# Optimization experiments

Measured on AMD Instinct MI355X. Metric: run time of the kernel, lower is better.

The kernel has to match this reference:

```python
import jax, jax.numpy as jnp
import numpy as np

B, T, H, L2 = 131072, 4, 8, 5  # T=4 forced by conv1 in_channels=4; L2 = layers 1..5 of the 6-layer lstm1


def _lstm_dir(xs, w_ih, w_hh, b, h0, c0):
    # xs: [T, B, Din] -> hs: [T, B, H]; PyTorch gate order i, f, g, o
    def step(carry, xt):
        h, c = carry
        g = xt @ w_ih.T + h @ w_hh.T + b
        i, f, gg, o = jnp.split(g, 4, axis=-1)
        c = jax.nn.sigmoid(f) * c + jax.nn.sigmoid(i) * jnp.tanh(gg)
        h = jax.nn.sigmoid(o) * jnp.tanh(c)
        return (h, c), h
    _, hs = jax.lax.scan(step, (h0, c0), xs)
    return hs


def _bilstm(xs, wi_f, wh_f, b_f, wi_b, wh_b, b_b, h0f, c0f, h0b, c0b):
    hf = _lstm_dir(xs, wi_f, wh_f, b_f, h0f, c0f)
    hb = _lstm_dir(xs[::-1], wi_b, wh_b, b_b, h0b, c0b)[::-1]
    return jnp.concatenate([hf, hb], axis=-1)  # [T, B, 2H]


def _conv1d(x, w, b):
    # x: [B, C, L], w: [O, I, K] (torch Conv1d layout)
    y = jax.lax.conv_general_dilated(x, w, (1,), [(0, 0)], dimension_numbers=('NCH', 'OIH', 'NCH'))
    return y + b[None, :, None]


def _deconv1d(x, w, b):
    # torch ConvTranspose1d weight [I, O, K]; stride 1, pad 0 == full conv with flipped kernel
    k = w.shape[-1]
    wk = jnp.flip(jnp.swapaxes(w, 0, 1), -1)  # [O, I, K]
    y = jax.lax.conv_general_dilated(x, wk, (1,), [(k - 1, k - 1)], dimension_numbers=('NCH', 'OIH', 'NCH'))
    return y + b[None, :, None]


def setup_inputs():
    key = jax.random.key(0)
    ks = iter(jax.random.split(key, 32))
    rn = lambda shape, s=0.2: jax.random.normal(next(ks), shape, jnp.float32) * s
    return {
        'x': rn((B, T, 2), 1.0),
        'h0': rn((12, B, H), 1.0),
        'c0': rn((12, B, H), 1.0),
        'w_ih0': rn((2, 4 * H, 2)),
        'w_hh0': rn((2, 4 * H, H)),
        'b_ih0': rn((2, 4 * H)),
        'b_hh0': rn((2, 4 * H)),
        'w_ih': rn((L2, 2, 4 * H, 2 * H)),
        'w_hh': rn((L2, 2, 4 * H, H)),
        'b_ih': rn((L2, 2, 4 * H)),
        'b_hh': rn((L2, 2, 4 * H)),
        'conv1_w': rn((8, 4, 2)), 'conv1_b': rn((8,)),
        'conv2_w': rn((16, 8, 2)), 'conv2_b': rn((16,)),
        'deconv1_w': rn((16, 8, 2)), 'deconv1_b': rn((8,)),
        'deconv2_w': rn((8, 4, 2)), 'deconv2_b': rn((4,)),
        'fc1_w': rn((8, 16)), 'fc1_b': rn((8,)),
        'fc2_w': rn((4, 8)), 'fc2_b': rn((4,)),
    }


def reference(x, h0, c0, w_ih0, w_hh0, b_ih0, b_hh0, w_ih, w_hh, b_ih, b_hh,
              conv1_w, conv1_b, conv2_w, conv2_b, deconv1_w, deconv1_b,
              deconv2_w, deconv2_b, fc1_w, fc1_b, fc2_w, fc2_b):
    xs = jnp.swapaxes(x, 0, 1)  # [T, B, 2]
    y = _bilstm(xs, w_ih0[0], w_hh0[0], b_ih0[0] + b_hh0[0],
                w_ih0[1], w_hh0[1], b_ih0[1] + b_hh0[1],
                h0[0], c0[0], h0[1], c0[1])
    for l in range(L2):  # fixed, small layer count (eval mode: inter-layer dropout off)
        i = 2 * (l + 1)
        y = _bilstm(y, w_ih[l, 0], w_hh[l, 0], b_ih[l, 0] + b_hh[l, 0],
                    w_ih[l, 1], w_hh[l, 1], b_ih[l, 1] + b_hh[l, 1],
                    h0[i], c0[i], h0[i + 1], c0[i + 1])
    y = jax.nn.sigmoid(jnp.swapaxes(y, 0, 1))  # [B, 4, 16]; dim 1 acts as conv channels
    y = _conv1d(y, conv1_w, conv1_b)           # [B, 8, 15]
    y = _conv1d(y, conv2_w, conv2_b)           # [B, 16, 14]
    y = _deconv1d(y, deconv1_w, deconv1_b)     # [B, 8, 15]
    y = _deconv1d(y, deconv2_w, deconv2_b)     # [B, 4, 16]
    y = y @ fc1_w.T + fc1_b                    # [B, 4, 8]
    y = y @ fc2_w.T + fc2_b                    # [B, 4, 4]
    return jnp.tanh(y)
```

## Files before the change

### kernel.cpp

```cpp
#include <hip/hip_runtime.h>
#include <hip/hip_bf16.h>


using f32x2 = __attribute__((ext_vector_type(2))) float;
using f32x4 = __attribute__((ext_vector_type(4))) float;

#define OFF_WIH0 0
#define OFF_WHH0 128
#define OFF_B0   640
#define OFF_WIH  704
#define OFF_WHH  5824
#define OFF_B    8384
#define OFF_M    9024
#define OFF_MB   10048

__device__ __forceinline__ float rcpf_(float x) {
#if __has_builtin(__builtin_amdgcn_rcpf)
    return __builtin_amdgcn_rcpf(x);
#else
    return 1.0f / x;
#endif
}
__device__ __forceinline__ float exp2f_(float x) {
#if __has_builtin(__builtin_amdgcn_exp2f)
    return __builtin_amdgcn_exp2f(x);
#else
    return exp2f(x);
#endif
}
__device__ __forceinline__ float sigm(float x) {
    return rcpf_(1.0f + exp2f_(-1.44269504f * x));
}
__device__ __forceinline__ float tanhx(float x) {
    return fmaf(2.0f, rcpf_(1.0f + exp2f_(-2.88539008f * x)), -1.0f);
}

__global__ __launch_bounds__(256) void prep_all(
    const float* __restrict__ wih0, const float* __restrict__ whh0,
    const float* __restrict__ bih0, const float* __restrict__ bhh0,
    const float* __restrict__ wih,  const float* __restrict__ whh,
    const float* __restrict__ bih,  const float* __restrict__ bhh,
    const float* __restrict__ c1w, const float* __restrict__ c1b,
    const float* __restrict__ c2w, const float* __restrict__ c2b,
    const float* __restrict__ d1w, const float* __restrict__ d1b,
    const float* __restrict__ d2w, const float* __restrict__ d2b,
    const float* __restrict__ f1w, const float* __restrict__ f1b,
    const float* __restrict__ f2w, const float* __restrict__ f2b,
    float* __restrict__ W)
{
    __shared__ float A[13][232];
    __shared__ float Bf[13][232];
    const int tid = threadIdx.x;

    if (blockIdx.x < 36) {
        int t = blockIdx.x * 256 + tid;
        const int n = 36 * 256;
        for (int i = t; i < 128; i += n)  W[OFF_WIH0 + i] = wih0[i];
        for (int i = t; i < 512; i += n)  W[OFF_WHH0 + i] = whh0[i];
        for (int i = t; i < 64; i += n)   W[OFF_B0 + i] = bih0[i] + bhh0[i];
        for (int i = t; i < 5120; i += n) W[OFF_WIH + i] = wih[i];
        for (int i = t; i < 2560; i += n) W[OFF_WHH + i] = whh[i];
        for (int i = t; i < 640; i += n)  W[OFF_B + i] = bih[i] + bhh[i];
        return;
    }
    const int base = (blockIdx.x - 36) * 13;

    for (int idx = tid; idx < 13 * 64; idx += 256) {
        int cl = idx / 64, r = idx % 64;
        A[cl][r] = (base + cl == r) ? 1.0f : 0.0f;
    }
    __syncthreads();
    for (int idx = tid; idx < 13 * 120; idx += 256) {
        int cl = idx / 120, rr = idx % 120; int o = rr / 15, l = rr % 15;
        float acc = (base + cl == 64) ? c1b[o] : 0.0f;
        for (int i = 0; i < 4; i++)
            for (int kk = 0; kk < 2; kk++)
                acc += c1w[(o * 4 + i) * 2 + kk] * A[cl][i * 16 + l + kk];
        Bf[cl][rr] = acc;
    }
    __syncthreads();
    for (int idx = tid; idx < 13 * 224; idx += 256) {
        int cl = idx / 224, rr = idx % 224; int o = rr / 14, l = rr % 14;
        float acc = (base + cl == 64) ? c2b[o] : 0.0f;
        for (int i = 0; i < 8; i++)
            for (int kk = 0; kk < 2; kk++)
                acc += c2w[(o * 8 + i) * 2 + kk] * Bf[cl][i * 15 + l + kk];
        A[cl][rr] = acc;
    }
    __syncthreads();
    for (int idx = tid; idx < 13 * 120; idx += 256) {
        int cl = idx / 120, rr = idx % 120; int o = rr / 15, l = rr % 15;
        float acc = (base + cl == 64) ? d1b[o] : 0.0f;
        for (int i = 0; i < 16; i++)
            for (int kk = 0; kk < 2; kk++) {
                int ls = l - kk;
                if (ls >= 0 && ls < 14)
                    acc += d1w[(i * 8 + o) * 2 + kk] * A[cl][i * 14 + ls];
            }
        Bf[cl][rr] = acc;
    }
    __syncthreads();
    for (int idx = tid; idx < 13 * 64; idx += 256) {
        int cl = idx / 64, rr = idx % 64; int o = rr / 16, l = rr % 16;
        float acc = (base + cl == 64) ? d2b[o] : 0.0f;
        for (int i = 0; i < 8; i++)
            for (int kk = 0; kk < 2; kk++) {
                int ls = l - kk;
                if (ls >= 0 && ls < 15)
                    acc += d2w[(i * 4 + o) * 2 + kk] * Bf[cl][i * 15 + ls];
            }
        A[cl][rr] = acc;
    }
    __syncthreads();
    for (int idx = tid; idx < 13 * 32; idx += 256) {
        int cl = idx / 32, rr = idx % 32; int ch = rr / 8, jj = rr % 8;
        float acc = (base + cl == 64) ? f1b[jj] : 0.0f;
        for (int l = 0; l < 16; l++)
            acc += f1w[jj * 16 + l] * A[cl][ch * 16 + l];
        Bf[cl][rr] = acc;
    }
    __syncthreads();
    for (int idx = tid; idx < 13 * 16; idx += 256) {
        int cl = idx / 16, rr = idx % 16; int ch = rr / 4, m = rr % 4;
        int col = base + cl;
        if (col > 64) continue;
        float acc = (col == 64) ? f2b[m] : 0.0f;
        for (int j = 0; j < 8; j++)
            acc += f2w[m * 8 + j] * Bf[cl][ch * 8 + j];
        if (col < 64) W[OFF_M + rr * 64 + col] = acc;
        else          W[OFF_MB + rr] = acc;
    }
}

template<bool FWD, bool LAST>
__device__ __forceinline__ void layer16(
    const float* __restrict__ Wi, const float* __restrict__ Wh,
    const float* __restrict__ Bs,
    const float* __restrict__ h0s, const float* __restrict__ c0s,
    int gelem0, int u,
    float* const (&lin)[2], float* const (&lout)[2])
{
    f32x4 wiv[4][4];
    f32x4 whv[4][2];
    f32x4 bsv;
#pragma unroll
    for (int g = 0; g < 4; g++) {
        const int r = u + 8 * g;
        const f32x4* wr = reinterpret_cast<const f32x4*>(Wi + r * 16);
        wiv[g][0] = wr[0]; wiv[g][1] = wr[1]; wiv[g][2] = wr[2]; wiv[g][3] = wr[3];
        const f32x4* ur = reinterpret_cast<const f32x4*>(Wh + r * 8);
        whv[g][0] = ur[0]; whv[g][1] = ur[1];
        bsv[g] = Bs[r];
    }
    f32x4 hg[2][2];
    float cc[2];
#pragma unroll
    for (int e = 0; e < 2; e++) {
        const f32x4* hp = reinterpret_cast<const f32x4*>(h0s + (size_t)(gelem0 + e) * 8);
        hg[e][0] = hp[0]; hg[e][1] = hp[1];
        cc[e] = c0s[(size_t)(gelem0 + e) * 8 + u];
    }
    float hreg[2][4];
    const int off = FWD ? 0 : 8;

#pragma unroll
    for (int s = 0; s < 4; s++) {
        const int t = FWD ? s : 3 - s;
        const int tprev = FWD ? t - 1 : t + 1;
        f32x2 acc[2][4];
#pragma unroll
        for (int e = 0; e < 2; e++) {
            const f32x4* ip = reinterpret_cast<const f32x4*>(lin[e] + 16 * t);
            f32x4 i0 = ip[0], i1 = ip[1], i2 = ip[2], i3 = ip[3];
            f32x4 ha, hb;
            if (s == 0) { ha = hg[e][0]; hb = hg[e][1]; }
            else {
                const f32x4* hp = reinterpret_cast<const f32x4*>(lout[e] + 16 * tprev + off);
                ha = hp[0]; hb = hp[1];
            }
            f32x2 xin[8];
            xin[0] = f32x2{i0.x, i0.y}; xin[1] = f32x2{i0.z, i0.w};
            xin[2] = f32x2{i1.x, i1.y}; xin[3] = f32x2{i1.z, i1.w};
            xin[4] = f32x2{i2.x, i2.y}; xin[5] = f32x2{i2.z, i2.w};
            xin[6] = f32x2{i3.x, i3.y}; xin[7] = f32x2{i3.z, i3.w};
            f32x2 hx[4];
            hx[0] = f32x2{ha.x, ha.y}; hx[1] = f32x2{ha.z, ha.w};
            hx[2] = f32x2{hb.x, hb.y}; hx[3] = f32x2{hb.z, hb.w};
#pragma unroll
            for (int g = 0; g < 4; g++) {
                f32x2 a = f32x2{bsv[g], 0.0f};
#pragma unroll
                for (int j = 0; j < 4; j++) {
                    f32x2 wlo = f32x2{wiv[g][j].x, wiv[g][j].y};
                    f32x2 whi = f32x2{wiv[g][j].z, wiv[g][j].w};
                    a = __builtin_elementwise_fma(xin[2 * j], wlo, a);
                    a = __builtin_elementwise_fma(xin[2 * j + 1], whi, a);
                }
#pragma unroll
                for (int j = 0; j < 2; j++) {
                    f32x2 wlo = f32x2{whv[g][j].x, whv[g][j].y};
                    f32x2 whi = f32x2{whv[g][j].z, whv[g][j].w};
                    a = __builtin_elementwise_fma(hx[2 * j], wlo, a);
                    a = __builtin_elementwise_fma(hx[2 * j + 1], whi, a);
                }
                acc[e][g] = a;
            }
        }
#pragma unroll
        for (int e = 0; e < 2; e++) {
            float si = sigm(acc[e][0].x + acc[e][0].y);
            float sf = sigm(acc[e][1].x + acc[e][1].y);
            float tg = tanhx(acc[e][2].x + acc[e][2].y);
            float so = sigm(acc[e][3].x + acc[e][3].y);
            cc[e] = fmaf(sf, cc[e], si * tg);
            float hn = so * tanhx(cc[e]);
            lout[e][16 * t + off + u] = hn;
            if (LAST) hreg[e][s] = hn;
        }
    }
    if (LAST) {
#pragma unroll
        for (int e = 0; e < 2; e++)
#pragma unroll
            for (int s = 0; s < 4; s++) {
                const int t = FWD ? s : 3 - s;
                lout[e][16 * t + off + u] = sigm(hreg[e][s]);
            }
    }
}

template<bool FWD>
__device__ __forceinline__ void layer2(
    const float* __restrict__ Wi, const float* __restrict__ Wh,
    const float* __restrict__ Bs,
    const float* __restrict__ h0s, const float* __restrict__ c0s,
    int gelem0, int u,
    const f32x2 (&xin2)[2][4], float* const (&lout)[2])
{
    f32x2 wiv[4];
    f32x4 whv[4][2];
    f32x4 bsv;
#pragma unroll
    for (int g = 0; g < 4; g++) {
        const int r = u + 8 * g;
        wiv[g] = *reinterpret_cast<const f32x2*>(Wi + r * 2);
        const f32x4* ur = reinterpret_cast<const f32x4*>(Wh + r * 8);
        whv[g][0] = ur[0]; whv[g][1] = ur[1];
        bsv[g] = Bs[r];
    }
    f32x4 hg[2][2];
    float cc[2];
#pragma unroll
    for (int e = 0; e < 2; e++) {
        const f32x4* hp = reinterpret_cast<const f32x4*>(h0s + (size_t)(gelem0 + e) * 8);
        hg[e][0] = hp[0]; hg[e][1] = hp[1];
        cc[e] = c0s[(size_t)(gelem0 + e) * 8 + u];
    }
    const int off = FWD ? 0 : 8;

#pragma unroll
    for (int s = 0; s < 4; s++) {
        const int t = FWD ? s : 3 - s;
        const int tprev = FWD ? t - 1 : t + 1;
        f32x2 acc[2][4];
#pragma unroll
        for (int e = 0; e < 2; e++) {
            f32x4 ha, hb;
            if (s == 0) { ha = hg[e][0]; hb = hg[e][1]; }
            else {
                const f32x4* hp = reinterpret_cast<const f32x4*>(lout[e] + 16 * tprev + off);
                ha = hp[0]; hb = hp[1];
            }
            f32x2 hx[4];
            hx[0] = f32x2{ha.x, ha.y}; hx[1] = f32x2{ha.z, ha.w};
            hx[2] = f32x2{hb.x, hb.y}; hx[3] = f32x2{hb.z, hb.w};
#pragma unroll
            for (int g = 0; g < 4; g++) {
                f32x2 a = __builtin_elementwise_fma(xin2[e][t], wiv[g], f32x2{bsv[g], 0.0f});
#pragma unroll
                for (int j = 0; j < 2; j++) {
                    f32x2 wlo = f32x2{whv[g][j].x, whv[g][j].y};
                    f32x2 whi = f32x2{whv[g][j].z, whv[g][j].w};
                    a = __builtin_elementwise_fma(hx[2 * j], wlo, a);
                    a = __builtin_elementwise_fma(hx[2 * j + 1], whi, a);
                }
                acc[e][g] = a;
            }
        }
#pragma unroll
        for (int e = 0; e < 2; e++) {
            float si = sigm(acc[e][0].x + acc[e][0].y);
            float sf = sigm(acc[e][1].x + acc[e][1].y);
            float tg = tanhx(acc[e][2].x + acc[e][2].y);
            float so = sigm(acc[e][3].x + acc[e][3].y);
            cc[e] = fmaf(sf, cc[e], si * tg);
            lout[e][16 * t + off + u] = so * tanhx(cc[e]);
        }
    }
}

__global__ __launch_bounds__(256, 3) void lstm_main(
    const float* __restrict__ x, const float* __restrict__ h0,
    const float* __restrict__ c0, const float* __restrict__ W,
    float* __restrict__ out, int B)
{
    __shared__ float yb[2][64 * 68];
    const int tid = threadIdx.x;
    const int u = tid & 7;
    const int slot = tid >> 3;
    const int row0 = slot * 2;
    const int gelem0 = blockIdx.x * 64 + row0;

    float* y0[2]; float* y1[2];
#pragma unroll
    for (int e = 0; e < 2; e++) {
        y0[e] = &yb[0][(row0 + e) * 68];
        y1[e] = &yb[1][(row0 + e) * 68];
    }

    f32x2 xin2[2][4];
#pragma unroll
    for (int e = 0; e < 2; e++) {
        const f32x4* xp = reinterpret_cast<const f32x4*>(x + (size_t)(gelem0 + e) * 8);
        f32x4 a = xp[0], b = xp[1];
        xin2[e][0] = f32x2{a.x, a.y}; xin2[e][1] = f32x2{a.z, a.w};
        xin2[e][2] = f32x2{b.x, b.y}; xin2[e][3] = f32x2{b.z, b.w};
    }

    layer2<true>(W + OFF_WIH0, W + OFF_WHH0, W + OFF_B0,
                 h0 + (size_t)0 * B * 8, c0 + (size_t)0 * B * 8,
                 gelem0, u, xin2, y0);
    layer2<false>(W + OFF_WIH0 + 64, W + OFF_WHH0 + 256, W + OFF_B0 + 32,
                  h0 + (size_t)1 * B * 8, c0 + (size_t)1 * B * 8,
                  gelem0, u, xin2, y0);

#pragma unroll
    for (int l = 1; l <= 4; l++) {
        float* const (&lin)[2] = (l & 1) ? y0 : y1;
        float* const (&lout)[2] = (l & 1) ? y1 : y0;
        const float* wi = W + OFF_WIH + (size_t)(l - 1) * 1024;
        const float* wh = W + OFF_WHH + (size_t)(l - 1) * 512;
        const float* bb = W + OFF_B + (size_t)(l - 1) * 64;
        const int si = 2 * l;
        layer16<true, false>(wi, wh, bb,
                             h0 + (size_t)si * B * 8, c0 + (size_t)si * B * 8,
                             gelem0, u, lin, lout);
        layer16<false, false>(wi + 512, wh + 256, bb + 32,
                              h0 + (size_t)(si + 1) * B * 8, c0 + (size_t)(si + 1) * B * 8,
                              gelem0, u, lin, lout);
    }
    {
        const float* wi = W + OFF_WIH + (size_t)4 * 1024;
        const float* wh = W + OFF_WHH + (size_t)4 * 512;
        const float* bb = W + OFF_B + (size_t)4 * 64;
        layer16<true, true>(wi, wh, bb,
                            h0 + (size_t)10 * B * 8, c0 + (size_t)10 * B * 8,
                            gelem0, u, y0, y1);
        layer16<false, true>(wi + 512, wh + 256, bb + 32,
                             h0 + (size_t)11 * B * 8, c0 + (size_t)11 * B * 8,
                             gelem0, u, y0, y1);
    }

    {
        const int o0 = 2 * u, o1 = 2 * u + 1;
        const f32x4* M0 = reinterpret_cast<const f32x4*>(W + OFF_M + o0 * 64);
        const f32x4* M1 = reinterpret_cast<const f32x4*>(W + OFF_M + o1 * 64);
        const float b0 = W[OFF_MB + o0];
        const float b1 = W[OFF_MB + o1];
#pragma unroll
        for (int e = 0; e < 2; e++) {
            float a0 = b0, a1 = b1;
#pragma unroll
            for (int q = 0; q < 16; q++) {
                f32x4 sv = *reinterpret_cast<const f32x4*>(y1[e] + 4 * q);
                f32x4 m0 = M0[q], m1 = M1[q];
                a0 = fmaf(sv.x, m0.x, a0); a0 = fmaf(sv.y, m0.y, a0);
                a0 = fmaf(sv.z, m0.z, a0); a0 = fmaf(sv.w, m0.w, a0);
                a1 = fmaf(sv.x, m1.x, a1); a1 = fmaf(sv.y, m1.y, a1);
                a1 = fmaf(sv.z, m1.z, a1); a1 = fmaf(sv.w, m1.w, a1);
            }
            f32x2 res;
            res.x = tanhx(a0);
            res.y = tanhx(a1);
            *reinterpret_cast<f32x2*>(out + (size_t)(gelem0 + e) * 16 + 2 * u) = res;
        }
    }
}

extern "C" void kernel_launch(void* const* d_in, const int* in_sizes, int n_in,
                              void* d_out, int out_size, void* d_ws, size_t ws_size,
                              hipStream_t stream)
{
    const float* x    = (const float*)d_in[0];
    const float* h0   = (const float*)d_in[1];
    const float* c0   = (const float*)d_in[2];
    const float* wih0 = (const float*)d_in[3];
    const float* whh0 = (const float*)d_in[4];
    const float* bih0 = (const float*)d_in[5];
    const float* bhh0 = (const float*)d_in[6];
    const float* wih  = (const float*)d_in[7];
    const float* whh  = (const float*)d_in[8];
    const float* bih  = (const float*)d_in[9];
    const float* bhh  = (const float*)d_in[10];
    const float* c1w  = (const float*)d_in[11];
    const float* c1b  = (const float*)d_in[12];
    const float* c2w  = (const float*)d_in[13];
    const float* c2b  = (const float*)d_in[14];
    const float* d1w  = (const float*)d_in[15];
    const float* d1b  = (const float*)d_in[16];
    const float* d2w  = (const float*)d_in[17];
    const float* d2b  = (const float*)d_in[18];
    const float* f1w  = (const float*)d_in[19];
    const float* f1b  = (const float*)d_in[20];
    const float* f2w  = (const float*)d_in[21];
    const float* f2b  = (const float*)d_in[22];

    float* W = (float*)d_ws;
    const int B = in_sizes[0] / 8;

    prep_all<<<41, 256, 0, stream>>>(wih0, whh0, bih0, bhh0, wih, whh, bih, bhh,
                                     c1w, c1b, c2w, c2b, d1w, d1b, d2w, d2b,
                                     f1w, f1b, f2w, f2b, W);
    lstm_main<<<B / 64, 256, 0, stream>>>(x, h0, c0, W, (float*)d_out, B);
}
```

Before: 345.1 us.

## Gather recurrent hidden state via DPP lane swizzles instead of LDS reloads

Each step's 8-wide hidden state was read back from shared memory. It is now assembled in registers with DPP cross-lane moves (quad_perm and row_shl patterns) among the 8 lanes that own a sequence. The recurrent weights and the initial h are loaded in the matching XOR-permuted order so each lane's FMAs line up with the swizzled values. This removes an LDS store-to-load dependency from the serial recurrence. Launch bounds also go from 3 to 4 blocks per CU, which trades registers for occupancy.

```diff
diff --git a/kernel.cpp b/kernel.cpp
--- a/kernel.cpp
+++ b/kernel.cpp
@@ -33,6 +33,22 @@
 }
 __device__ __forceinline__ float tanhx(float x) {
     return fmaf(2.0f, rcpf_(1.0f + exp2f_(-2.88539008f * x)), -1.0f);
+}
+
+template<int CTRL>
+__device__ __forceinline__ float dppf(float x) {
+    return __builtin_bit_cast(float, __builtin_amdgcn_update_dpp(
+        0, __builtin_bit_cast(int, x), CTRL, 0xF, 0xF, true));
+}
+__device__ __forceinline__ void hgather(float hn, f32x2 (&hx)[4]) {
+    float v0 = hn;
+    float v1 = dppf<0xB1>(v0);
+    float v2 = dppf<0x4E>(v0);
+    float v3 = dppf<0x4E>(v1);
+    hx[0] = f32x2{v0, v1};
+    hx[1] = f32x2{v2, v3};
+    hx[2] = f32x2{dppf<0x141>(v0), dppf<0x141>(v1)};
+    hx[3] = f32x2{dppf<0x141>(v2), dppf<0x141>(v3)};
 }
 
 __global__ __launch_bounds__(256) void prep_all(
@@ -141,23 +157,29 @@
     float* const (&lin)[2], float* const (&lout)[2])
 {
     f32x4 wiv[4][4];
-    f32x4 whv[4][2];
+    f32x2 whp[4][4];
     f32x4 bsv;
 #pragma unroll
     for (int g = 0; g < 4; g++) {
         const int r = u + 8 * g;
         const f32x4* wr = reinterpret_cast<const f32x4*>(Wi + r * 16);
         wiv[g][0] = wr[0]; wiv[g][1] = wr[1]; wiv[g][2] = wr[2]; wiv[g][3] = wr[3];
-        const f32x4* ur = reinterpret_cast<const f32x4*>(Wh + r * 8);
-        whv[g][0] = ur[0]; whv[g][1] = ur[1];
+        const float* uw = Wh + r * 8;
+        whp[g][0] = f32x2{uw[u],     uw[u ^ 1]};
+        whp[g][1] = f32x2{uw[u ^ 2], uw[u ^ 3]};
+        whp[g][2] = f32x2{uw[u ^ 7], uw[u ^ 6]};
+        whp[g][3] = f32x2{uw[u ^ 5], uw[u ^ 4]};
         bsv[g] = Bs[r];
     }
-    f32x4 hg[2][2];
+    f32x2 hx[2][4];
     float cc[2];
 #pragma unroll
     for (int e = 0; e < 2; e++) {
-        const f32x4* hp = reinterpret_cast<const f32x4*>(h0s + (size_t)(gelem0 + e) * 8);
-        hg[e][0] = hp[0]; hg[e][1] = hp[1];
+        const float* hp = h0s + (size_t)(gelem0 + e) * 8;
+        hx[e][0] = f32x2{hp[u],     hp[u ^ 1]};
+        hx[e][1] = f32x2{hp[u ^ 2], hp[u ^ 3]};
+        hx[e][2] = f32x2{hp[u ^ 7], hp[u ^ 6]};
+        hx[e][3] = f32x2{hp[u ^ 5], hp[u ^ 4]};
         cc[e] = c0s[(size_t)(gelem0 + e) * 8 + u];
     }
     float hreg[2][4];
@@ -166,26 +188,16 @@
 #pragma unroll
     for (int s = 0; s < 4; s++) {
         const int t = FWD ? s : 3 - s;
-        const int tprev = FWD ? t - 1 : t + 1;
         f32x2 acc[2][4];
 #pragma unroll
         for (int e = 0; e < 2; e++) {
             const f32x4* ip = reinterpret_cast<const f32x4*>(lin[e] + 16 * t);
             f32x4 i0 = ip[0], i1 = ip[1], i2 = ip[2], i3 = ip[3];
-            f32x4 ha, hb;
-            if (s == 0) { ha = hg[e][0]; hb = hg[e][1]; }
-            else {
-                const f32x4* hp = reinterpret_cast<const f32x4*>(lout[e] + 16 * tprev + off);
-                ha = hp[0]; hb = hp[1];
-            }
             f32x2 xin[8];
             xin[0] = f32x2{i0.x, i0.y}; xin[1] = f32x2{i0.z, i0.w};
             xin[2] = f32x2{i1.x, i1.y}; xin[3] = f32x2{i1.z, i1.w};
             xin[4] = f32x2{i2.x, i2.y}; xin[5] = f32x2{i2.z, i2.w};
             xin[6] = f32x2{i3.x, i3.y}; xin[7] = f32x2{i3.z, i3.w};
-            f32x2 hx[4];
-            hx[0] = f32x2{ha.x, ha.y}; hx[1] = f32x2{ha.z, ha.w};
-            hx[2] = f32x2{hb.x, hb.y}; hx[3] = f32x2{hb.z, hb.w};
 #pragma unroll
             for (int g = 0; g < 4; g++) {
                 f32x2 a = f32x2{bsv[g], 0.0f};
@@ -197,12 +209,8 @@
                     a = __builtin_elementwise_fma(xin[2 * j + 1], whi, a);
                 }
 #pragma unroll
-                for (int j = 0; j < 2; j++) {
-                    f32x2 wlo = f32x2{whv[g][j].x, whv[g][j].y};
-                    f32x2 whi = f32x2{whv[g][j].z, whv[g][j].w};
-                    a = __builtin_elementwise_fma(hx[2 * j], wlo, a);
-                    a = __builtin_elementwise_fma(hx[2 * j + 1], whi, a);
-                }
+                for (int k = 0; k < 4; k++)
+                    a = __builtin_elementwise_fma(hx[e][k], whp[g][k], a);
                 acc[e][g] = a;
             }
         }
@@ -215,6 +223,7 @@
             cc[e] = fmaf(sf, cc[e], si * tg);
             float hn = so * tanhx(cc[e]);
             lout[e][16 * t + off + u] = hn;
+            if (s < 3) hgather(hn, hx[e]);
             if (LAST) hreg[e][s] = hn;
         }
     }
@@ -238,22 +247,28 @@
     const f32x2 (&xin2)[2][4], float* const (&lout)[2])
 {
     f32x2 wiv[4];
-    f32x4 whv[4][2];
+    f32x2 whp[4][4];
     f32x4 bsv;
 #pragma unroll
     for (int g = 0; g < 4; g++) {
         const int r = u + 8 * g;
         wiv[g] = *reinterpret_cast<const f32x2*>(Wi + r * 2);
-        const f32x4* ur = reinterpret_cast<const f32x4*>(Wh + r * 8);
-        whv[g][0] = ur[0]; whv[g][1] = ur[1];
+        const float* uw = Wh + r * 8;
+        whp[g][0] = f32x2{uw[u],     uw[u ^ 1]};
+        whp[g][1] = f32x2{uw[u ^ 2], uw[u ^ 3]};
+        whp[g][2] = f32x2{uw[u ^ 7], uw[u ^ 6]};
+        whp[g][3] = f32x2{uw[u ^ 5], uw[u ^ 4]};
         bsv[g] = Bs[r];
     }
-    f32x4 hg[2][2];
+    f32x2 hx[2][4];
     float cc[2];
 #pragma unroll
     for (int e = 0; e < 2; e++) {
-        const f32x4* hp = reinterpret_cast<const f32x4*>(h0s + (size_t)(gelem0 + e) * 8);
-        hg[e][0] = hp[0]; hg[e][1] = hp[1];
+        const float* hp = h0s + (size_t)(gelem0 + e) * 8;
+        hx[e][0] = f32x2{hp[u],     hp[u ^ 1]};
+        hx[e][1] = f32x2{hp[u ^ 2], hp[u ^ 3]};
+        hx[e][2] = f32x2{hp[u ^ 7], hp[u ^ 6]};
+        hx[e][3] = f32x2{hp[u ^ 5], hp[u ^ 4]};
         cc[e] = c0s[(size_t)(gelem0 + e) * 8 + u];
     }
     const int off = FWD ? 0 : 8;
@@ -261,29 +276,15 @@
 #pragma unroll
     for (int s = 0; s < 4; s++) {
         const int t = FWD ? s : 3 - s;
-        const int tprev = FWD ? t - 1 : t + 1;
         f32x2 acc[2][4];
 #pragma unroll
         for (int e = 0; e < 2; e++) {
-            f32x4 ha, hb;
-            if (s == 0) { ha = hg[e][0]; hb = hg[e][1]; }
-            else {
-                const f32x4* hp = reinterpret_cast<const f32x4*>(lout[e] + 16 * tprev + off);
-                ha = hp[0]; hb = hp[1];
-            }
-            f32x2 hx[4];
-            hx[0] = f32x2{ha.x, ha.y}; hx[1] = f32x2{ha.z, ha.w};
-            hx[2] = f32x2{hb.x, hb.y}; hx[3] = f32x2{hb.z, hb.w};
 #pragma unroll
             for (int g = 0; g < 4; g++) {
                 f32x2 a = __builtin_elementwise_fma(xin2[e][t], wiv[g], f32x2{bsv[g], 0.0f});
 #pragma unroll
-                for (int j = 0; j < 2; j++) {
-                    f32x2 wlo = f32x2{whv[g][j].x, whv[g][j].y};
-                    f32x2 whi = f32x2{whv[g][j].z, whv[g][j].w};
-                    a = __builtin_elementwise_fma(hx[2 * j], wlo, a);
-                    a = __builtin_elementwise_fma(hx[2 * j + 1], whi, a);
-                }
+                for (int k = 0; k < 4; k++)
+                    a = __builtin_elementwise_fma(hx[e][k], whp[g][k], a);
                 acc[e][g] = a;
             }
         }
@@ -294,12 +295,14 @@
             float tg = tanhx(acc[e][2].x + acc[e][2].y);
             float so = sigm(acc[e][3].x + acc[e][3].y);
             cc[e] = fmaf(sf, cc[e], si * tg);
-            lout[e][16 * t + off + u] = so * tanhx(cc[e]);
+            float hn = so * tanhx(cc[e]);
+            lout[e][16 * t + off + u] = hn;
+            if (s < 3) hgather(hn, hx[e]);
         }
     }
 }
 
-__global__ __launch_bounds__(256, 3) void lstm_main(
+__global__ __launch_bounds__(256, 4) void lstm_main(
     const float* __restrict__ x, const float* __restrict__ h0,
     const float* __restrict__ c0, const float* __restrict__ W,
     float* __restrict__ out, int B)
```

Result: slower. 894.1 us (+159.1%).

## Run forward and backward LSTM directions concurrently on separate thread groups

Applied to the files above, without the earlier changes.

Each slot of 16 threads now splits into two 8-thread groups, one per LSTM direction. The two directions of every bidirectional layer run at the same time instead of one after the other inside each thread. Each block handles 32 batch rows instead of 64, so the grid doubles while the shared buffer and the per-thread serial recurrence chain are halved. The final projection has each thread compute one output column instead of two. Because the two direction groups of a slot sit in the same wavefront, no extra barrier is added; in exchange, output stores become scalar and per-block weight loads are duplicated across twice as many blocks.

```diff
diff --git a/kernel.cpp b/kernel.cpp
--- a/kernel.cpp
+++ b/kernel.cpp
@@ -132,12 +132,12 @@
     }
 }
 
-template<bool FWD, bool LAST>
-__device__ __forceinline__ void layer16(
+template<bool LAST>
+__device__ __forceinline__ void layer16d(
     const float* __restrict__ Wi, const float* __restrict__ Wh,
     const float* __restrict__ Bs,
     const float* __restrict__ h0s, const float* __restrict__ c0s,
-    int gelem0, int u,
+    int gelem0, int u, int toff, int off,
     float* const (&lin)[2], float* const (&lout)[2])
 {
     f32x4 wiv[4][4];
@@ -161,12 +161,11 @@
         cc[e] = c0s[(size_t)(gelem0 + e) * 8 + u];
     }
     float hreg[2][4];
-    const int off = FWD ? 0 : 8;
 
 #pragma unroll
     for (int s = 0; s < 4; s++) {
-        const int t = FWD ? s : 3 - s;
-        const int tprev = FWD ? t - 1 : t + 1;
+        const int t = s ^ toff;
+        const int tprev = (s - 1) ^ toff;
         f32x2 acc[2][4];
 #pragma unroll
         for (int e = 0; e < 2; e++) {
@@ -223,18 +222,17 @@
         for (int e = 0; e < 2; e++)
 #pragma unroll
             for (int s = 0; s < 4; s++) {
-                const int t = FWD ? s : 3 - s;
+                const int t = s ^ toff;
                 lout[e][16 * t + off + u] = sigm(hreg[e][s]);
             }
     }
 }
 
-template<bool FWD>
-__device__ __forceinline__ void layer2(
+__device__ __forceinline__ void layer2d(
     const float* __restrict__ Wi, const float* __restrict__ Wh,
     const float* __restrict__ Bs,
     const float* __restrict__ h0s, const float* __restrict__ c0s,
-    int gelem0, int u,
+    int gelem0, int u, int toff, int off,
     const f32x2 (&xin2)[2][4], float* const (&lout)[2])
 {
     f32x2 wiv[4];
@@ -256,15 +254,15 @@
         hg[e][0] = hp[0]; hg[e][1] = hp[1];
         cc[e] = c0s[(size_t)(gelem0 + e) * 8 + u];
     }
-    const int off = FWD ? 0 : 8;
 
 #pragma unroll
     for (int s = 0; s < 4; s++) {
-        const int t = FWD ? s : 3 - s;
-        const int tprev = FWD ? t - 1 : t + 1;
+        const int t = s ^ toff;
+        const int tprev = (s - 1) ^ toff;
         f32x2 acc[2][4];
 #pragma unroll
         for (int e = 0; e < 2; e++) {
+            f32x2 xv = toff ? xin2[e][3 - s] : xin2[e][s];
             f32x4 ha, hb;
             if (s == 0) { ha = hg[e][0]; hb = hg[e][1]; }
             else {
@@ -276,7 +274,7 @@
             hx[2] = f32x2{hb.x, hb.y}; hx[3] = f32x2{hb.z, hb.w};
 #pragma unroll
             for (int g = 0; g < 4; g++) {
-                f32x2 a = __builtin_elementwise_fma(xin2[e][t], wiv[g], f32x2{bsv[g], 0.0f});
+                f32x2 a = __builtin_elementwise_fma(xv, wiv[g], f32x2{bsv[g], 0.0f});
 #pragma unroll
                 for (int j = 0; j < 2; j++) {
                     f32x2 wlo = f32x2{whv[g][j].x, whv[g][j].y};
@@ -304,12 +302,16 @@
     const float* __restrict__ c0, const float* __restrict__ W,
     float* __restrict__ out, int B)
 {
-    __shared__ float yb[2][64 * 68];
+    __shared__ float yb[2][32 * 68];
     const int tid = threadIdx.x;
     const int u = tid & 7;
-    const int slot = tid >> 3;
+    const int dir = (tid >> 3) & 1;
+    const int slot = tid >> 4;
     const int row0 = slot * 2;
-    const int gelem0 = blockIdx.x * 64 + row0;
+    const int gelem0 = blockIdx.x * 32 + row0;
+    const int toff = dir ? 3 : 0;
+    const int off  = dir ? 8 : 0;
+    const size_t B8 = (size_t)B * 8;
 
     float* y0[2]; float* y1[2];
 #pragma unroll
@@ -327,62 +329,47 @@
         xin2[e][2] = f32x2{b.x, b.y}; xin2[e][3] = f32x2{b.z, b.w};
     }
 
-    layer2<true>(W + OFF_WIH0, W + OFF_WHH0, W + OFF_B0,
-                 h0 + (size_t)0 * B * 8, c0 + (size_t)0 * B * 8,
-                 gelem0, u, xin2, y0);
-    layer2<false>(W + OFF_WIH0 + 64, W + OFF_WHH0 + 256, W + OFF_B0 + 32,
-                  h0 + (size_t)1 * B * 8, c0 + (size_t)1 * B * 8,
-                  gelem0, u, xin2, y0);
+    layer2d(W + OFF_WIH0 + dir * 64, W + OFF_WHH0 + dir * 256, W + OFF_B0 + dir * 32,
+            h0 + (size_t)(0 + dir) * B8, c0 + (size_t)(0 + dir) * B8,
+            gelem0, u, toff, off, xin2, y0);
 
 #pragma unroll
     for (int l = 1; l <= 4; l++) {
         float* const (&lin)[2] = (l & 1) ? y0 : y1;
         float* const (&lout)[2] = (l & 1) ? y1 : y0;
-        const float* wi = W + OFF_WIH + (size_t)(l - 1) * 1024;
-        const float* wh = W + OFF_WHH + (size_t)(l - 1) * 512;
-        const float* bb = W + OFF_B + (size_t)(l - 1) * 64;
-        const int si = 2 * l;
-        layer16<true, false>(wi, wh, bb,
-                             h0 + (size_t)si * B * 8, c0 + (size_t)si * B * 8,
-                             gelem0, u, lin, lout);
-        layer16<false, false>(wi + 512, wh + 256, bb + 32,
-                              h0 + (size_t)(si + 1) * B * 8, c0 + (size_t)(si + 1) * B * 8,
-                              gelem0, u, lin, lout);
+        const float* wi = W + OFF_WIH + (size_t)(l - 1) * 1024 + dir * 512;
+        const float* wh = W + OFF_WHH + (size_t)(l - 1) * 512 + dir * 256;
+        const float* bb = W + OFF_B + (size_t)(l - 1) * 64 + dir * 32;
+        const int si = 2 * l + dir;
+        layer16d<false>(wi, wh, bb,
+                        h0 + (size_t)si * B8, c0 + (size_t)si * B8,
+                        gelem0, u, toff, off, lin, lout);
     }
     {
-        const float* wi = W + OFF_WIH + (size_t)4 * 1024;
-        const float* wh = W + OFF_WHH + (size_t)4 * 512;
-        const float* bb = W + OFF_B + (size_t)4 * 64;
-        layer16<true, true>(wi, wh, bb,
-                            h0 + (size_t)10 * B * 8, c0 + (size_t)10 * B * 8,
-                            gelem0, u, y0, y1);
-        layer16<false, true>(wi + 512, wh + 256, bb + 32,
-                             h0 + (size_t)11 * B * 8, c0 + (size_t)11 * B * 8,
-                             gelem0, u, y0, y1);
+        const float* wi = W + OFF_WIH + (size_t)4 * 1024 + dir * 512;
+        const float* wh = W + OFF_WHH + (size_t)4 * 512 + dir * 256;
+        const float* bb = W + OFF_B + (size_t)4 * 64 + dir * 32;
+        const int si = 10 + dir;
+        layer16d<true>(wi, wh, bb,
+                       h0 + (size_t)si * B8, c0 + (size_t)si * B8,
+                       gelem0, u, toff, off, y0, y1);
     }
 
     {
-        const int o0 = 2 * u, o1 = 2 * u + 1;
-        const f32x4* M0 = reinterpret_cast<const f32x4*>(W + OFF_M + o0 * 64);
-        const f32x4* M1 = reinterpret_cast<const f32x4*>(W + OFF_M + o1 * 64);
-        const float b0 = W[OFF_MB + o0];
-        const float b1 = W[OFF_MB + o1];
+        const int o = off + u;
+        const f32x4* Mr = reinterpret_cast<const f32x4*>(W + OFF_M + o * 64);
+        const float bo = W[OFF_MB + o];
 #pragma unroll
         for (int e = 0; e < 2; e++) {
-            float a0 = b0, a1 = b1;
+            float a0 = bo;
 #pragma unroll
             for (int q = 0; q < 16; q++) {
                 f32x4 sv = *reinterpret_cast<const f32x4*>(y1[e] + 4 * q);
-                f32x4 m0 = M0[q], m1 = M1[q];
+                f32x4 m0 = Mr[q];
                 a0 = fmaf(sv.x, m0.x, a0); a0 = fmaf(sv.y, m0.y, a0);
                 a0 = fmaf(sv.z, m0.z, a0); a0 = fmaf(sv.w, m0.w, a0);
-                a1 = fmaf(sv.x, m1.x, a1); a1 = fmaf(sv.y, m1.y, a1);
-                a1 = fmaf(sv.z, m1.z, a1); a1 = fmaf(sv.w, m1.w, a1);
-            }
-            f32x2 res;
-            res.x = tanhx(a0);
-            res.y = tanhx(a1);
-            *reinterpret_cast<f32x2*>(out + (size_t)(gelem0 + e) * 16 + 2 * u) = res;
+            }
+            out[(size_t)(gelem0 + e) * 16 + o] = tanhx(a0);
         }
     }
 }
@@ -421,5 +408,5 @@
     prep_all<<<41, 256, 0, stream>>>(wih0, whh0, bih0, bhh0, wih, whh, bih, bhh,
                                      c1w, c1b, c2w, c2b, d1w, d1b, d2w, d2b,
                                      f1w, f1b, f2w, f2b, W);
-    lstm_main<<<B / 64, 256, 0, stream>>>(x, h0, c0, W, (float*)d_out, B);
-}
+    lstm_main<<<B / 32, 256, 0, stream>>>(x, h0, c0, W, (float*)d_out, B);
+}
```

New measurement: 459.0 us. 1.33x slower.
